# Kernel tuning notes

Hardware: AMD Instinct MI355X
Metric: run time of the kernel (lower is better)

Reference implementation:

```python
import jax, jax.numpy as jnp
import numpy as np

D_EMB = 768
N_HEADS = 12
D_K = D_EMB // N_HEADS


def setup_inputs() -> dict:
    key = jax.random.key(0)
    k0, k1, k2, k3, k4 = jax.random.split(key, 5)
    B, S = 2, 4096
    scale = 1.0 / np.sqrt(D_EMB)
    return {
        "inputs": jax.random.normal(k0, (B, S, D_EMB), dtype=jnp.float32),
        "Wq": jax.random.normal(k1, (D_EMB, D_EMB), dtype=jnp.float32) * scale,
        "Wk": jax.random.normal(k2, (D_EMB, D_EMB), dtype=jnp.float32) * scale,
        "Wv": jax.random.normal(k3, (D_EMB, D_EMB), dtype=jnp.float32) * scale,
        "Wo": jax.random.normal(k4, (D_EMB, D_EMB), dtype=jnp.float32) * scale,
    }


def reference(inputs, Wq, Wk, Wv, Wo):
    B, S, _ = inputs.shape
    def split_heads(x):  # [B,S,E] -> [B,H,S,dk]
        return x.reshape(B, S, N_HEADS, D_K).transpose(0, 2, 1, 3)
    q = split_heads(inputs @ Wq)
    k = split_heads(inputs @ Wk)
    v = split_heads(inputs @ Wv)
    scores = jnp.einsum("bhqd,bhkd->bhqk", q, k) / jnp.sqrt(
        jnp.asarray(D_K, dtype=inputs.dtype)
    )
    attn = jax.nn.softmax(scores, axis=-1)
    out = jnp.einsum("bhqk,bhkd->bhqd", attn, v)
    out = out.transpose(0, 2, 1, 3).reshape(B, S, D_EMB)
    return out @ Wo
```

## Files before the change

kernel.cpp:

```cpp
#include <hip/hip_runtime.h>

#define D_EMB 768
#define NH 12
#define DK 64
#define NB 2
#define SS 4096
#define E3 (3*D_EMB)
#define MM (NB*SS)

typedef unsigned short u16;
typedef __attribute__((ext_vector_type(8))) __bf16 bf16x8;
typedef __attribute__((ext_vector_type(4))) float f32x4;
typedef __attribute__((ext_vector_type(4))) unsigned int u32x4;

static __device__ __forceinline__ u16 f2bf(float f) {
  unsigned u = __builtin_bit_cast(unsigned, f);
  u += 0x7fffu + ((u >> 16) & 1u);
  return (u16)(u >> 16);
}
static __device__ __forceinline__ f32x4 mfma16(bf16x8 a, bf16x8 b, f32x4 c) {
  return __builtin_amdgcn_mfma_f32_16x16x32_bf16(a, b, c, 0, 0, 0);
}
static __device__ __forceinline__ float exp2_fast(float x) {
#if __has_builtin(__builtin_amdgcn_exp2f)
  return __builtin_amdgcn_exp2f(x);
#else
  return __builtin_exp2f(x);
#endif
}
static __device__ __forceinline__ float rcp_fast(float x) {
#if __has_builtin(__builtin_amdgcn_rcpf)
  return __builtin_amdgcn_rcpf(x);
#else
  return 1.f / x;
#endif
}
static __device__ __forceinline__ void gload_lds16(const u16* g, u16* l) {
  __builtin_amdgcn_global_load_lds((const __attribute__((address_space(1))) void*)g,
                                   (__attribute__((address_space(3))) void*)l, 16, 0, 0);
}

__global__ __launch_bounds__(256) void cast_kernel(const float* __restrict__ in,
                                                   u16* __restrict__ out, int n) {
  int i = (blockIdx.x * 256 + threadIdx.x) * 4;
  if (i + 3 < n) {
    float4 v = *(const float4*)(in + i);
    out[i + 0] = f2bf(v.x);
    out[i + 1] = f2bf(v.y);
    out[i + 2] = f2bf(v.z);
    out[i + 3] = f2bf(v.w);
  }
}

__global__ __launch_bounds__(256) void transpose_cast_all(const float* __restrict__ Wq,
                                                          const float* __restrict__ Wk,
                                                          const float* __restrict__ Wv,
                                                          const float* __restrict__ Wo,
                                                          u16* __restrict__ WTqkv,
                                                          u16* __restrict__ WoT, float qscale) {
  __shared__ float tile[32][33];
  int z = blockIdx.z;
  const float* W = (z == 0) ? Wq : (z == 1) ? Wk : (z == 2) ? Wv : Wo;
  u16* WT = (z < 3) ? WTqkv + (size_t)z * D_EMB * D_EMB : WoT;
  float scale = (z == 0) ? qscale : 1.0f;
  int kb = blockIdx.y * 32, nb = blockIdx.x * 32;
  int tx = threadIdx.x, ty = threadIdx.y;
#pragma unroll
  for (int i = 0; i < 4; i++)
    tile[ty + i * 8][tx] = W[(size_t)(kb + ty + i * 8) * D_EMB + nb + tx];
  __syncthreads();
#pragma unroll
  for (int i = 0; i < 4; i++)
    WT[(size_t)(nb + ty + i * 8) * D_EMB + kb + tx] = f2bf(tile[tx][ty + i * 8] * scale);
}

__global__ __launch_bounds__(256) void transpose_v(const u16* __restrict__ QKV,
                                                   u16* __restrict__ VT) {
  __shared__ u16 tile[32][33];
  int bh = blockIdx.z;
  int b = bh / NH, h = bh % NH;
  int sb = blockIdx.x * 32, db = blockIdx.y * 32;
  int tx = threadIdx.x, ty = threadIdx.y;
  const u16* src = QKV + (size_t)(b * SS) * E3 + 2 * D_EMB + h * DK;
  u16* dst = VT + (size_t)bh * DK * SS;
#pragma unroll
  for (int i = 0; i < 4; i++)
    tile[ty + i * 8][tx] = src[(size_t)(sb + ty + i * 8) * E3 + db + tx];
  __syncthreads();
  int s = sb + tx;
  int k6 = s & 63;
  int p = (s & ~63) | (k6 & 0x23) | ((k6 & 0x0C) << 1) | ((k6 & 0x10) >> 2);
#pragma unroll
  for (int i = 0; i < 4; i++)
    dst[(size_t)(db + ty + i * 8) * SS + p] = tile[tx][ty + i * 8];
}

template <int OUTF32>
__global__ __launch_bounds__(256) void gemm_bt(const u16* __restrict__ A,
                                               const u16* __restrict__ Bt,
                                               void* __restrict__ Cout,
                                               int M, int N, int K, float scale) {
  __shared__ __align__(16) u16 As[2 * 128 * 64];
  __shared__ __align__(16) u16 Bs[2 * 128 * 64];
  int tid = threadIdx.x;
  int wave = tid >> 6, lane = tid & 63;
  int g = lane >> 4, nIdx = lane & 15;
  int m0 = blockIdx.y * 128, n0 = blockIdx.x * 128;
  int wm = (wave >> 1) * 64, wn = (wave & 1) * 64;

  f32x4 acc[4][4] = {};

  int rL = lane >> 3, cL = lane & 7;
  int xr8 = (cL ^ rL) * 8;
  int xrn = nIdx & 7;
  int nk = K >> 6;

#pragma unroll
  for (int i = 0; i < 4; i++) {
    int r = (wave * 4 + i) * 8 + rL;
    gload_lds16(A  + (size_t)(m0 + r) * K + xr8,
                As + (wave * 4 + i) * 512 + lane * 8);
    gload_lds16(Bt + (size_t)(n0 + r) * K + xr8,
                Bs + (wave * 4 + i) * 512 + lane * 8);
  }

  for (int kt = 0; kt < nk; kt++) {
    __syncthreads();

    int cb = (kt & 1) * 8192;

    if (kt + 1 < nk) {
      int nb = ((kt + 1) & 1) * 8192;
      int k0n = (kt + 1) << 6;
#pragma unroll
      for (int i = 0; i < 4; i++) {
        int r = (wave * 4 + i) * 8 + rL;
        gload_lds16(A  + (size_t)(m0 + r) * K + k0n + xr8,
                    As + nb + (wave * 4 + i) * 512 + lane * 8);
        gload_lds16(Bt + (size_t)(n0 + r) * K + k0n + xr8,
                    Bs + nb + (wave * 4 + i) * 512 + lane * 8);
      }
    }

#pragma unroll
    for (int ks = 0; ks < 2; ks++) {
      bf16x8 af[4], bfr[4];
#pragma unroll
      for (int i = 0; i < 4; i++)
        af[i] = *(const bf16x8*)(As + cb + (wm + i * 16 + nIdx) * 64 + ((ks * 4 + g) ^ xrn) * 8);
#pragma unroll
      for (int j = 0; j < 4; j++)
        bfr[j] = *(const bf16x8*)(Bs + cb + (wn + j * 16 + nIdx) * 64 + ((ks * 4 + g) ^ xrn) * 8);
#pragma unroll
      for (int i = 0; i < 4; i++)
#pragma unroll
        for (int j = 0; j < 4; j++)
          acc[i][j] = mfma16(af[i], bfr[j], acc[i][j]);
    }
  }

#pragma unroll
  for (int i = 0; i < 4; i++)
#pragma unroll
    for (int j = 0; j < 4; j++)
#pragma unroll
      for (int r = 0; r < 4; r++) {
        int rr = m0 + wm + i * 16 + g * 4 + r;
        int cc = n0 + wn + j * 16 + nIdx;
        float v = acc[i][j][r] * scale;
        if (OUTF32)
          ((float*)Cout)[(size_t)rr * N + cc] = v;
        else
          ((u16*)Cout)[(size_t)rr * N + cc] = f2bf(v);
      }
}

__global__ __launch_bounds__(256, 2) void flash(const u16* __restrict__ QKV,
                                                const u16* __restrict__ VT,
                                                u16* __restrict__ O) {
  __shared__ __align__(16) u16 smem[32768];

  int b = blockIdx.z, h = blockIdx.y;
  int q0 = blockIdx.x * 128;
  int tid = threadIdx.x, w = tid >> 6, l = tid & 63;
  int g = l >> 4, n = l & 15;
  int qh = w & 1, st = w >> 1;

  const u16* VTb = VT + (size_t)(b * NH + h) * DK * SS;
  u16* sbase = smem + st * 16384;

  const u16* Qbase = QKV + (size_t)(b * SS + q0 + qh * 64) * E3 + h * DK;
  bf16x8 qf[4][2];
#pragma unroll
  for (int qg = 0; qg < 4; qg++)
#pragma unroll
    for (int hf = 0; hf < 2; hf++)
      qf[qg][hf] = *(const bf16x8*)(Qbase + (size_t)(qg * 16 + n) * E3 + hf * 32 + g * 8);

  f32x4 o_acc[4][4] = {};
  float lsum[4] = {0.f, 0.f, 0.f, 0.f};
  u32x4 onev = {0x3F803F80u, 0x3F803F80u, 0x3F803F80u, 0x3F803F80u};
  bf16x8 aone = __builtin_bit_cast(bf16x8, onev);

  int rL = l >> 3, cL = l & 7;
  int xr8 = (cL ^ rL) * 8;
  const u16* g0;
  size_t rstep, tstep;
  u16* sd0;
  if ((w & 1) == 0) {
    g0 = QKV + ((size_t)(b * SS) + st * 2048 + rL) * E3 + D_EMB + h * DK + xr8;
    rstep = (size_t)8 * E3;
    tstep = (size_t)64 * E3;
    sd0 = sbase + l * 8;
  } else {
    g0 = VTb + (size_t)rL * SS + st * 2048 + xr8;
    rstep = (size_t)8 * SS;
    tstep = 64;
    sd0 = sbase + 4096 + l * 8;
  }

#pragma unroll
  for (int i = 0; i < 8; i++)
    gload_lds16(g0 + i * rstep, sd0 + i * 512);

  int xrn = (n & 7);
  for (int kt = 0; kt < 32; kt++) {
    __syncthreads();

    const u16* pK = sbase + (kt & 1) * 8192;
    const u16* pV = pK + 4096;

    if (kt < 31) {
      const u16* gn = g0 + (size_t)(kt + 1) * tstep;
      u16* sd = sd0 + ((kt + 1) & 1) * 8192;
#pragma unroll
      for (int i = 0; i < 8; i++)
        gload_lds16(gn + i * rstep, sd + i * 512);
    }

#pragma unroll
    for (int s = 0; s < 2; s++) {
      bf16x8 kf[2][2];
#pragma unroll
      for (int jj = 0; jj < 2; jj++)
#pragma unroll
        for (int hf = 0; hf < 2; hf++)
          kf[jj][hf] = *(const bf16x8*)(pK + ((2 * s + jj) * 16 + n) * 64 +
                                        ((hf * 4 + g) ^ xrn) * 8);

#pragma unroll
      for (int p = 0; p < 2; p++) {
        f32x4 C[2][2];
#pragma unroll
        for (int q2 = 0; q2 < 2; q2++) {
          int qg = 2 * p + q2;
#pragma unroll
          for (int jj = 0; jj < 2; jj++) {
            f32x4 t = {};
            t = mfma16(kf[jj][0], qf[qg][0], t);
            t = mfma16(kf[jj][1], qf[qg][1], t);
            C[q2][jj] = t;
          }
        }
        u32x4 Bw[2];
#pragma unroll
        for (int q2 = 0; q2 < 2; q2++)
#pragma unroll
          for (int jj = 0; jj < 2; jj++) {
            float p0 = exp2_fast(C[q2][jj][0]);
            float p1 = exp2_fast(C[q2][jj][1]);
            float p2 = exp2_fast(C[q2][jj][2]);
            float p3 = exp2_fast(C[q2][jj][3]);
            Bw[q2][jj * 2] = __builtin_amdgcn_perm(__builtin_bit_cast(unsigned, p1),
                                                   __builtin_bit_cast(unsigned, p0), 0x07060302u);
            Bw[q2][jj * 2 + 1] = __builtin_amdgcn_perm(__builtin_bit_cast(unsigned, p3),
                                                       __builtin_bit_cast(unsigned, p2), 0x07060302u);
          }
#pragma unroll
        for (int q2 = 0; q2 < 2; q2++) {
          f32x4 z = {};
          z = mfma16(aone, __builtin_bit_cast(bf16x8, Bw[q2]), z);
          lsum[2 * p + q2] += z[0];
        }
#pragma unroll
        for (int dt = 0; dt < 4; dt++) {
          bf16x8 vf = *(const bf16x8*)(pV + (dt * 16 + n) * 64 +
                                       ((s * 4 + g) ^ xrn) * 8);
#pragma unroll
          for (int q2 = 0; q2 < 2; q2++)
            o_acc[2 * p + q2][dt] = mfma16(vf, __builtin_bit_cast(bf16x8, Bw[q2]),
                                           o_acc[2 * p + q2][dt]);
        }
      }
    }
  }

  __syncthreads();

  float* dumpF = (float*)smem;
  if (w >= 2) {
    float* dst = dumpF + ((size_t)((w - 2) * 64 + l)) * 68;
#pragma unroll
    for (int qg = 0; qg < 4; qg++)
#pragma unroll
      for (int dt = 0; dt < 4; dt++)
        *(f32x4*)(dst + (qg * 4 + dt) * 4) = o_acc[qg][dt];
    f32x4 lv = {lsum[0], lsum[1], lsum[2], lsum[3]};
    *(f32x4*)(dst + 64) = lv;
  }
  __syncthreads();
  if (w < 2) {
    float* src = dumpF + ((size_t)(w * 64 + l)) * 68;
#pragma unroll
    for (int qg = 0; qg < 4; qg++)
#pragma unroll
      for (int dt = 0; dt < 4; dt++)
        o_acc[qg][dt] += *(f32x4*)(src + (qg * 4 + dt) * 4);
    f32x4 lv = *(f32x4*)(src + 64);
#pragma unroll
    for (int qg = 0; qg < 4; qg++) {
      float rl = rcp_fast(lsum[qg] + lv[qg]);
      u16* Obp = O + (size_t)(b * SS + q0 + w * 64 + qg * 16 + n) * D_EMB + h * DK;
#pragma unroll
      for (int dt = 0; dt < 4; dt++) {
        uint2 pk;
        pk.x = (unsigned)f2bf(o_acc[qg][dt][0] * rl) |
               ((unsigned)f2bf(o_acc[qg][dt][1] * rl) << 16);
        pk.y = (unsigned)f2bf(o_acc[qg][dt][2] * rl) |
               ((unsigned)f2bf(o_acc[qg][dt][3] * rl) << 16);
        *(uint2*)(Obp + dt * 16 + g * 4) = pk;
      }
    }
  }
}

extern "C" void kernel_launch(void* const* d_in, const int* in_sizes, int n_in,
                              void* d_out, int out_size, void* d_ws, size_t ws_size,
                              hipStream_t stream) {
  const float* X  = (const float*)d_in[0];
  const float* Wq = (const float*)d_in[1];
  const float* Wk = (const float*)d_in[2];
  const float* Wv = (const float*)d_in[3];
  const float* Wo = (const float*)d_in[4];
  float* out = (float*)d_out;

  u16* Xb    = (u16*)d_ws;
  u16* WTqkv = Xb + (size_t)MM * D_EMB;
  u16* WoT   = WTqkv + (size_t)E3 * D_EMB;
  u16* QKV   = WoT + (size_t)D_EMB * D_EMB;
  u16* VT    = QKV + (size_t)MM * E3;
  u16* Ob    = VT + (size_t)NB * NH * DK * SS;

  dim3 tb(32, 8);
  cast_kernel<<<(MM * D_EMB) / 1024, 256, 0, stream>>>(X, Xb, MM * D_EMB);
  transpose_cast_all<<<dim3(24, 24, 4), tb, 0, stream>>>(Wq, Wk, Wv, Wo, WTqkv, WoT,
                                                         0.125f * 1.4426950408889634f);
  gemm_bt<0><<<dim3(E3 / 128, MM / 128), 256, 0, stream>>>(Xb, WTqkv, (void*)QKV,
                                                           MM, E3, D_EMB, 1.0f);
  transpose_v<<<dim3(SS / 32, 2, NB * NH), tb, 0, stream>>>(QKV, VT);
  flash<<<dim3(SS / 128, NH, NB), 256, 0, stream>>>(QKV, VT, Ob);
  gemm_bt<1><<<dim3(D_EMB / 128, MM / 128), 256, 0, stream>>>(Ob, WoT, (void*)out,
                                                              MM, D_EMB, D_EMB, 1.0f);
}
```

Baseline: 255.2 us.

## Split flash attention over query rows instead of key halves, drop cross-wave reduction

Each of the four waves now owns 32 query rows and walks the full key sequence, where before two waves split the keys and merged partial results. All four waves cooperatively load one shared double-buffered K/V tile per step, halving LDS use and removing the final shared-memory reduction and its syncs. This halves per-wave accumulator registers but doubles the number of barrier-synchronised iterations, and each wave reuses each loaded K fragment over fewer query rows.

```diff
diff --git a/kernel.cpp b/kernel.cpp
--- a/kernel.cpp
+++ b/kernel.cpp
@@ -178,64 +178,63 @@
 __global__ __launch_bounds__(256, 2) void flash(const u16* __restrict__ QKV,
                                                 const u16* __restrict__ VT,
                                                 u16* __restrict__ O) {
-  __shared__ __align__(16) u16 smem[32768];
+  __shared__ __align__(16) u16 smem[16384];
 
   int b = blockIdx.z, h = blockIdx.y;
   int q0 = blockIdx.x * 128;
   int tid = threadIdx.x, w = tid >> 6, l = tid & 63;
   int g = l >> 4, n = l & 15;
-  int qh = w & 1, st = w >> 1;
 
   const u16* VTb = VT + (size_t)(b * NH + h) * DK * SS;
-  u16* sbase = smem + st * 16384;
-
-  const u16* Qbase = QKV + (size_t)(b * SS + q0 + qh * 64) * E3 + h * DK;
-  bf16x8 qf[4][2];
-#pragma unroll
-  for (int qg = 0; qg < 4; qg++)
+
+  const u16* Qbase = QKV + (size_t)(b * SS + q0 + w * 32) * E3 + h * DK;
+  bf16x8 qf[2][2];
+#pragma unroll
+  for (int qg = 0; qg < 2; qg++)
 #pragma unroll
     for (int hf = 0; hf < 2; hf++)
       qf[qg][hf] = *(const bf16x8*)(Qbase + (size_t)(qg * 16 + n) * E3 + hf * 32 + g * 8);
 
-  f32x4 o_acc[4][4] = {};
-  float lsum[4] = {0.f, 0.f, 0.f, 0.f};
+  f32x4 o_acc[2][4] = {};
+  float lsum[2] = {0.f, 0.f};
   u32x4 onev = {0x3F803F80u, 0x3F803F80u, 0x3F803F80u, 0x3F803F80u};
   bf16x8 aone = __builtin_bit_cast(bf16x8, onev);
 
-  int rL = l >> 3, cL = l & 7;
-  int xr8 = (cL ^ rL) * 8;
+  int t = tid & 127;
+  int rT = t >> 3, cT = t & 7;
+  int xr8 = (cT ^ (rT & 7)) * 8;
   const u16* g0;
   size_t rstep, tstep;
   u16* sd0;
-  if ((w & 1) == 0) {
-    g0 = QKV + ((size_t)(b * SS) + st * 2048 + rL) * E3 + D_EMB + h * DK + xr8;
-    rstep = (size_t)8 * E3;
+  if (w < 2) {
+    g0 = QKV + ((size_t)(b * SS) + rT) * E3 + D_EMB + h * DK + xr8;
+    rstep = (size_t)16 * E3;
     tstep = (size_t)64 * E3;
-    sd0 = sbase + l * 8;
+    sd0 = smem + t * 8;
   } else {
-    g0 = VTb + (size_t)rL * SS + st * 2048 + xr8;
-    rstep = (size_t)8 * SS;
+    g0 = VTb + (size_t)rT * SS + xr8;
+    rstep = (size_t)16 * SS;
     tstep = 64;
-    sd0 = sbase + 4096 + l * 8;
-  }
-
-#pragma unroll
-  for (int i = 0; i < 8; i++)
-    gload_lds16(g0 + i * rstep, sd0 + i * 512);
+    sd0 = smem + 8192 + t * 8;
+  }
+
+#pragma unroll
+  for (int i = 0; i < 4; i++)
+    gload_lds16(g0 + i * rstep, sd0 + i * 1024);
 
   int xrn = (n & 7);
-  for (int kt = 0; kt < 32; kt++) {
+  for (int kt = 0; kt < 64; kt++) {
     __syncthreads();
 
-    const u16* pK = sbase + (kt & 1) * 8192;
-    const u16* pV = pK + 4096;
-
-    if (kt < 31) {
+    const u16* pK = smem + (kt & 1) * 4096;
+    const u16* pV = smem + 8192 + (kt & 1) * 4096;
+
+    if (kt < 63) {
       const u16* gn = g0 + (size_t)(kt + 1) * tstep;
-      u16* sd = sd0 + ((kt + 1) & 1) * 8192;
-#pragma unroll
-      for (int i = 0; i < 8; i++)
-        gload_lds16(gn + i * rstep, sd + i * 512);
+      u16* sd = sd0 + ((kt + 1) & 1) * 4096;
+#pragma unroll
+      for (int i = 0; i < 4; i++)
+        gload_lds16(gn + i * rstep, sd + i * 1024);
     }
 
 #pragma unroll
@@ -248,88 +247,60 @@
           kf[jj][hf] = *(const bf16x8*)(pK + ((2 * s + jj) * 16 + n) * 64 +
                                         ((hf * 4 + g) ^ xrn) * 8);
 
-#pragma unroll
-      for (int p = 0; p < 2; p++) {
-        f32x4 C[2][2];
-#pragma unroll
-        for (int q2 = 0; q2 < 2; q2++) {
-          int qg = 2 * p + q2;
-#pragma unroll
-          for (int jj = 0; jj < 2; jj++) {
-            f32x4 t = {};
-            t = mfma16(kf[jj][0], qf[qg][0], t);
-            t = mfma16(kf[jj][1], qf[qg][1], t);
-            C[q2][jj] = t;
-          }
+      f32x4 C[2][2];
+#pragma unroll
+      for (int q2 = 0; q2 < 2; q2++)
+#pragma unroll
+        for (int jj = 0; jj < 2; jj++) {
+          f32x4 tacc = {};
+          tacc = mfma16(kf[jj][0], qf[q2][0], tacc);
+          tacc = mfma16(kf[jj][1], qf[q2][1], tacc);
+          C[q2][jj] = tacc;
         }
-        u32x4 Bw[2];
+      u32x4 Bw[2];
+#pragma unroll
+      for (int q2 = 0; q2 < 2; q2++)
+#pragma unroll
+        for (int jj = 0; jj < 2; jj++) {
+          float p0 = exp2_fast(C[q2][jj][0]);
+          float p1 = exp2_fast(C[q2][jj][1]);
+          float p2 = exp2_fast(C[q2][jj][2]);
+          float p3 = exp2_fast(C[q2][jj][3]);
+          Bw[q2][jj * 2] = __builtin_amdgcn_perm(__builtin_bit_cast(unsigned, p1),
+                                                 __builtin_bit_cast(unsigned, p0), 0x07060302u);
+          Bw[q2][jj * 2 + 1] = __builtin_amdgcn_perm(__builtin_bit_cast(unsigned, p3),
+                                                     __builtin_bit_cast(unsigned, p2), 0x07060302u);
+        }
+#pragma unroll
+      for (int q2 = 0; q2 < 2; q2++) {
+        f32x4 z = {};
+        z = mfma16(aone, __builtin_bit_cast(bf16x8, Bw[q2]), z);
+        lsum[q2] += z[0];
+      }
+#pragma unroll
+      for (int dt = 0; dt < 4; dt++) {
+        bf16x8 vf = *(const bf16x8*)(pV + (dt * 16 + n) * 64 +
+                                     ((s * 4 + g) ^ xrn) * 8);
 #pragma unroll
         for (int q2 = 0; q2 < 2; q2++)
-#pragma unroll
-          for (int jj = 0; jj < 2; jj++) {
-            float p0 = exp2_fast(C[q2][jj][0]);
-            float p1 = exp2_fast(C[q2][jj][1]);
-            float p2 = exp2_fast(C[q2][jj][2]);
-            float p3 = exp2_fast(C[q2][jj][3]);
-            Bw[q2][jj * 2] = __builtin_amdgcn_perm(__builtin_bit_cast(unsigned, p1),
-                                                   __builtin_bit_cast(unsigned, p0), 0x07060302u);
-            Bw[q2][jj * 2 + 1] = __builtin_amdgcn_perm(__builtin_bit_cast(unsigned, p3),
-                                                       __builtin_bit_cast(unsigned, p2), 0x07060302u);
-          }
-#pragma unroll
-        for (int q2 = 0; q2 < 2; q2++) {
-          f32x4 z = {};
-          z = mfma16(aone, __builtin_bit_cast(bf16x8, Bw[q2]), z);
-          lsum[2 * p + q2] += z[0];
-        }
-#pragma unroll
-        for (int dt = 0; dt < 4; dt++) {
-          bf16x8 vf = *(const bf16x8*)(pV + (dt * 16 + n) * 64 +
-                                       ((s * 4 + g) ^ xrn) * 8);
-#pragma unroll
-          for (int q2 = 0; q2 < 2; q2++)
-            o_acc[2 * p + q2][dt] = mfma16(vf, __builtin_bit_cast(bf16x8, Bw[q2]),
-                                           o_acc[2 * p + q2][dt]);
-        }
+          o_acc[q2][dt] = mfma16(vf, __builtin_bit_cast(bf16x8, Bw[q2]),
+                                 o_acc[q2][dt]);
       }
     }
   }
 
-  __syncthreads();
-
-  float* dumpF = (float*)smem;
-  if (w >= 2) {
-    float* dst = dumpF + ((size_t)((w - 2) * 64 + l)) * 68;
-#pragma unroll
-    for (int qg = 0; qg < 4; qg++)
-#pragma unroll
-      for (int dt = 0; dt < 4; dt++)
-        *(f32x4*)(dst + (qg * 4 + dt) * 4) = o_acc[qg][dt];
-    f32x4 lv = {lsum[0], lsum[1], lsum[2], lsum[3]};
-    *(f32x4*)(dst + 64) = lv;
-  }
-  __syncthreads();
-  if (w < 2) {
-    float* src = dumpF + ((size_t)(w * 64 + l)) * 68;
-#pragma unroll
-    for (int qg = 0; qg < 4; qg++)
-#pragma unroll
-      for (int dt = 0; dt < 4; dt++)
-        o_acc[qg][dt] += *(f32x4*)(src + (qg * 4 + dt) * 4);
-    f32x4 lv = *(f32x4*)(src + 64);
-#pragma unroll
-    for (int qg = 0; qg < 4; qg++) {
-      float rl = rcp_fast(lsum[qg] + lv[qg]);
-      u16* Obp = O + (size_t)(b * SS + q0 + w * 64 + qg * 16 + n) * D_EMB + h * DK;
-#pragma unroll
-      for (int dt = 0; dt < 4; dt++) {
-        uint2 pk;
-        pk.x = (unsigned)f2bf(o_acc[qg][dt][0] * rl) |
-               ((unsigned)f2bf(o_acc[qg][dt][1] * rl) << 16);
-        pk.y = (unsigned)f2bf(o_acc[qg][dt][2] * rl) |
-               ((unsigned)f2bf(o_acc[qg][dt][3] * rl) << 16);
-        *(uint2*)(Obp + dt * 16 + g * 4) = pk;
-      }
+#pragma unroll
+  for (int qg = 0; qg < 2; qg++) {
+    float rl = rcp_fast(lsum[qg]);
+    u16* Obp = O + (size_t)(b * SS + q0 + w * 32 + qg * 16 + n) * D_EMB + h * DK;
+#pragma unroll
+    for (int dt = 0; dt < 4; dt++) {
+      uint2 pk;
+      pk.x = (unsigned)f2bf(o_acc[qg][dt][0] * rl) |
+             ((unsigned)f2bf(o_acc[qg][dt][1] * rl) << 16);
+      pk.y = (unsigned)f2bf(o_acc[qg][dt][2] * rl) |
+             ((unsigned)f2bf(o_acc[qg][dt][3] * rl) << 16);
+      *(uint2*)(Obp + dt * 16 + g * 4) = pk;
     }
   }
 }
```

Result: slower. 262.6 us (+2.9%).
